# Optimization experiments

Hardware: AMD Instinct MI355X
Metric: run time of the kernel (lower is better)

The kernel has to match this reference:

```python
import jax, jax.numpy as jnp
import numpy as np

B, C, H, W = 8, 512, 64, 32
SE_MID = C // 16
BN_EPS = 1e-5


def conv1x1(x, w, b):
    # x: [B,Cin,H,W], w: [Cout,Cin], b: [Cout]
    return jnp.einsum('bchw,oc->bohw', x, w) + b[None, :, None, None]


def setup_inputs() -> dict:
    key = jax.random.key(0)
    ks = jax.random.split(key, 17)
    s = 0.05
    return {
        'x': jax.random.normal(ks[0], (B, C, H, W), jnp.float32),
        'g_w': jax.random.normal(ks[1], (1, C), jnp.float32) * s,
        'g_b': jax.random.normal(ks[2], (1,), jnp.float32) * s,
        'theta_w': jax.random.normal(ks[3], (1, C), jnp.float32) * s,
        'theta_b': jax.random.normal(ks[4], (1,), jnp.float32) * s,
        'phi_w': jax.random.normal(ks[5], (1, C), jnp.float32) * s,
        'phi_b': jax.random.normal(ks[6], (1,), jnp.float32) * s,
        'W_w': jax.random.normal(ks[7], (C, 1), jnp.float32) * s,
        'W_b': jax.random.normal(ks[8], (C,), jnp.float32) * s,
        'bn_gamma': jax.random.normal(ks[9], (C,), jnp.float32) * s + 1.0,
        'bn_beta': jax.random.normal(ks[10], (C,), jnp.float32) * s,
        'bn_mean': jax.random.normal(ks[11], (C,), jnp.float32) * s,
        'bn_var': jax.random.uniform(ks[12], (C,), jnp.float32, 0.5, 1.5),
        'se1_w': jax.random.normal(ks[13], (SE_MID, C), jnp.float32) * s,
        'se1_b': jnp.zeros((SE_MID,), jnp.float32),
        'se2_w': jax.random.normal(ks[14], (C, SE_MID), jnp.float32) * s,
        'se2_b': jnp.zeros((C,), jnp.float32),
    }


def reference(x, g_w, g_b, theta_w, theta_b, phi_w, phi_b, W_w, W_b,
              bn_gamma, bn_beta, bn_mean, bn_var, se1_w, se1_b, se2_w, se2_b):
    b, c, h, w = x.shape
    N = h * w
    # SE channel gate from global average pool: [B,C,1,1]
    x_avg = jnp.mean(x, axis=(2, 3), keepdims=True)
    se_mid = jax.nn.relu(conv1x1(x_avg, se1_w, se1_b))
    W_cw = jax.nn.sigmoid(conv1x1(se_mid, se2_w, se2_b))  # [B,C,1,1]

    # inter_channels == 1: each projection is a length-N vector per sample
    g_x = conv1x1(x, g_w, g_b).reshape(b, N)          # [B,N]
    theta_x = conv1x1(x, theta_w, theta_b).reshape(b, N)  # [B,N]
    phi_x = conv1x1(x, phi_w, phi_b).reshape(b, N)        # [B,N]

    # f[b,i,j] = theta[b,i] * phi[b,j]; row softmax over j; y = f_div_C @ g
    f = theta_x[:, :, None] * phi_x[:, None, :]       # [B,N,N]
    f_div_C = jax.nn.softmax(f, axis=-1)
    y = jnp.einsum('bij,bj->bi', f_div_C, g_x)        # [B,N]
    y = y.reshape(b, 1, h, w)

    # W: 1x1 conv (1 -> C) + BatchNorm2d (inference form with running stats)
    W_y = conv1x1(y, W_w, W_b)                        # [B,C,H,W]
    inv = bn_gamma / jnp.sqrt(bn_var + BN_EPS)
    W_y = (W_y - bn_mean[None, :, None, None]) * inv[None, :, None, None] \
          + bn_beta[None, :, None, None]

    return W_cw * W_y + x
```

## Files before the change

### kernel.cpp

```cpp
#include <hip/hip_runtime.h>

#define BB 8
#define CC 512
#define NN 2048
#define SEM 32
#define BN_EPS 1e-5f
#define LOG2E 1.4426950408889634f

#define CG 32
#define NG (CC / CG)
#define KARR (NG * BB * NN)

__global__ __launch_bounds__(256) void k1(const float* __restrict__ x,
    const float* __restrict__ gw, const float* __restrict__ tw, const float* __restrict__ pw,
    float* __restrict__ pp, float* __restrict__ avgp)
{
    int tid = threadIdx.x;
    int wave = tid >> 6, lane = tid & 63;
    int blk = blockIdx.x;
    int h = blk & 1;
    int g = (blk >> 1) & (NG - 1);
    int b = blk >> 5;
    int c0 = g * CG;

    const float2* xp = reinterpret_cast<const float2*>(x)
                     + (size_t)(b * CC + c0) * (NN / 2) + h * 512 + tid;

    float2 ag0 = {0,0}, at0 = {0,0}, ap0 = {0,0};
    float2 ag1 = {0,0}, at1 = {0,0}, ap1 = {0,0};
    float s[CG];

    #pragma unroll 8
    for (int c = 0; c < CG; ++c) {
        float2 v0 = xp[(size_t)c * (NN / 2)];
        float2 v1 = xp[(size_t)c * (NN / 2) + 256];
        float wg = gw[c0 + c], wt = tw[c0 + c], wp = pw[c0 + c];
        ag0.x = fmaf(wg, v0.x, ag0.x); ag0.y = fmaf(wg, v0.y, ag0.y);
        at0.x = fmaf(wt, v0.x, at0.x); at0.y = fmaf(wt, v0.y, at0.y);
        ap0.x = fmaf(wp, v0.x, ap0.x); ap0.y = fmaf(wp, v0.y, ap0.y);
        ag1.x = fmaf(wg, v1.x, ag1.x); ag1.y = fmaf(wg, v1.y, ag1.y);
        at1.x = fmaf(wt, v1.x, at1.x); at1.y = fmaf(wt, v1.y, at1.y);
        ap1.x = fmaf(wp, v1.x, ap1.x); ap1.y = fmaf(wp, v1.y, ap1.y);
        s[c] = (v0.x + v0.y) + (v1.x + v1.y);
    }

    size_t i0 = (size_t)(g * BB + b) * 1024 + h * 512 + tid;
    float2* pp2 = reinterpret_cast<float2*>(pp);
    pp2[i0]                  = ag0;
    pp2[i0 + 256]            = ag1;
    pp2[KARR / 2 + i0]       = at0;
    pp2[KARR / 2 + i0 + 256] = at1;
    pp2[KARR + i0]           = ap0;
    pp2[KARR + i0 + 256]     = ap1;

    #pragma unroll
    for (int o = 32; o > 0; o >>= 1) {
        #pragma unroll
        for (int c = 0; c < CG; ++c) s[c] += __shfl_down(s[c], o);
    }
    if (lane == 0) {
        #pragma unroll
        for (int c = 0; c < CG; ++c)
            avgp[(size_t)(b * CC + c0 + c) * 8 + h * 4 + wave] = s[c];
    }
}

__global__ __launch_bounds__(256) void k2(
    const float* __restrict__ pp,
    const float* __restrict__ tb, const float* __restrict__ pb,
    float* __restrict__ gx, float* __restrict__ tx, float* __restrict__ px)
{
    int tid = threadIdx.x;
    int oct = blockIdx.x & 7;
    int g3  = blockIdx.x >> 3;
    int k   = g3 % 3;
    int b   = g3 / 3;
    int p   = oct * 256 + tid;
    const float* base = pp + (size_t)k * KARR + (size_t)b * NN + p;
    float v = 0.f;
    #pragma unroll
    for (int g = 0; g < NG; ++g)
        v += base[(size_t)g * BB * NN];
    int o = b * NN + p;
    if (k == 0)      gx[o] = v;
    else if (k == 1) tx[o] = v + tb[0];
    else             px[o] = v + pb[0];
}

__global__ __launch_bounds__(256) void k3(
    const float* __restrict__ gx, const float* __restrict__ tx,
    const float* __restrict__ px, const float* __restrict__ avgp,
    const float* __restrict__ gb,
    const float* __restrict__ se1w, const float* __restrict__ se1b,
    const float* __restrict__ se2w, const float* __restrict__ se2b,
    const float* __restrict__ Ww, const float* __restrict__ Wb,
    const float* __restrict__ gamma, const float* __restrict__ beta,
    const float* __restrict__ mean, const float* __restrict__ var,
    float* __restrict__ y, float* __restrict__ Ac, float* __restrict__ Dc)
{
    __shared__ float smem[4096];
    int tid = threadIdx.x;

    if (blockIdx.x >= 1024) {
        int b = blockIdx.x - 1024;
        float* sA = smem;
        float* sP = smem + 512;
        float* sM = smem + 768;
        for (int c = tid; c < CC; c += 256) {
            const float* apt = avgp + (size_t)(b * CC + c) * 8;
            float ssum = 0.f;
            #pragma unroll
            for (int k = 0; k < 8; ++k) ssum += apt[k];
            sA[c] = ssum * (1.0f / NN);
        }
        __syncthreads();
        {
            int m = tid >> 3, sub = tid & 7;
            const float* w1 = se1w + m * CC + sub * 64;
            const float* a1 = sA + sub * 64;
            float ssum = 0.f;
            #pragma unroll
            for (int k = 0; k < 64; ++k) ssum = fmaf(a1[k], w1[k], ssum);
            sP[m * 8 + sub] = ssum;
        }
        __syncthreads();
        if (tid < SEM) {
            float t = 0.f;
            #pragma unroll
            for (int k = 0; k < 8; ++k) t += sP[tid * 8 + k];
            sM[tid] = fmaxf(t + se1b[tid], 0.f);
        }
        __syncthreads();
        float gbv = gb[0];
        for (int c = tid; c < CC; c += 256) {
            float s2 = 0.f;
            #pragma unroll
            for (int m = 0; m < SEM; ++m) s2 = fmaf(sM[m], se2w[c * SEM + m], s2);
            s2 += se2b[c];
            float wcw = 1.f / (1.f + __expf(-s2));
            float inv = gamma[c] * rsqrtf(var[c] + BN_EPS);
            float A = wcw * Ww[c] * inv;
            Ac[b * CC + c] = A;
            Dc[b * CC + c] = wcw * ((Wb[c] - mean[c]) * inv + beta[c]) + A * gbv;
        }
        return;
    }

    float* spx = smem;
    float* sgx = smem + 2048;
    int b  = blockIdx.x >> 7;
    int i0 = (blockIdx.x & 127) << 4;
    {
        const float4* pxr = reinterpret_cast<const float4*>(px + (size_t)b * NN);
        const float4* gxr = reinterpret_cast<const float4*>(gx + (size_t)b * NN);
        float4* spx4 = reinterpret_cast<float4*>(spx);
        float4* sgx4 = reinterpret_cast<float4*>(sgx);
        #pragma unroll
        for (int w = 0; w < 2; ++w) {
            int idx = w * 256 + tid;
            spx4[idx] = pxr[idx];
            sgx4[idx] = gxr[idx];
        }
    }
    __syncthreads();

    int wave = tid >> 6, lane = tid & 63;
    int r0 = i0 + wave * 4;
    float t0 = tx[b * NN + r0 + 0] * LOG2E;
    float t1 = tx[b * NN + r0 + 1] * LOG2E;
    float t2 = tx[b * NN + r0 + 2] * LOG2E;
    float t3 = tx[b * NN + r0 + 3] * LOG2E;
    float s0 = 0.f, g0 = 0.f, s1 = 0.f, g1 = 0.f;
    float s2 = 0.f, g2 = 0.f, s3 = 0.f, g3 = 0.f;
    const float2* spx2 = reinterpret_cast<const float2*>(spx);
    const float2* sgx2 = reinterpret_cast<const float2*>(sgx);
    #pragma unroll 4
    for (int it = 0; it < 16; ++it) {
        int jj = it * 64 + lane;
        float2 xv = spx2[jj];
        float2 gv = sgx2[jj];
        float e0a = exp2f(fminf(t0 * xv.x, 115.f)), e0b = exp2f(fminf(t0 * xv.y, 115.f));
        float e1a = exp2f(fminf(t1 * xv.x, 115.f)), e1b = exp2f(fminf(t1 * xv.y, 115.f));
        float e2a = exp2f(fminf(t2 * xv.x, 115.f)), e2b = exp2f(fminf(t2 * xv.y, 115.f));
        float e3a = exp2f(fminf(t3 * xv.x, 115.f)), e3b = exp2f(fminf(t3 * xv.y, 115.f));
        s0 += e0a + e0b; g0 = fmaf(e0a, gv.x, fmaf(e0b, gv.y, g0));
        s1 += e1a + e1b; g1 = fmaf(e1a, gv.x, fmaf(e1b, gv.y, g1));
        s2 += e2a + e2b; g2 = fmaf(e2a, gv.x, fmaf(e2b, gv.y, g2));
        s3 += e3a + e3b; g3 = fmaf(e3a, gv.x, fmaf(e3b, gv.y, g3));
    }
    for (int o = 32; o > 0; o >>= 1) {
        s0 += __shfl_down(s0, o); g0 += __shfl_down(g0, o);
        s1 += __shfl_down(s1, o); g1 += __shfl_down(g1, o);
        s2 += __shfl_down(s2, o); g2 += __shfl_down(g2, o);
        s3 += __shfl_down(s3, o); g3 += __shfl_down(g3, o);
    }
    if (lane == 0) {
        y[b * NN + r0 + 0] = g0 / s0;
        y[b * NN + r0 + 1] = g1 / s1;
        y[b * NN + r0 + 2] = g2 / s2;
        y[b * NN + r0 + 3] = g3 / s3;
    }
}

__global__ __launch_bounds__(256) void k4(
    const float* __restrict__ x, const float* __restrict__ y,
    const float* __restrict__ Ac, const float* __restrict__ Dc,
    float* __restrict__ out)
{
    int bc = blockIdx.x;
    int b = bc >> 9;
    float a = Ac[bc], d = Dc[bc];
    const float4* x4 = reinterpret_cast<const float4*>(x) + (size_t)bc * (NN / 4);
    const float4* y4 = reinterpret_cast<const float4*>(y) + (size_t)b * (NN / 4);
    float4* o4 = reinterpret_cast<float4*>(out) + (size_t)bc * (NN / 4);
    int tid = threadIdx.x;
    #pragma unroll
    for (int k = 0; k < 2; ++k) {
        int idx = k * 256 + tid;
        float4 xv = x4[idx], yv = y4[idx], ov;
        ov.x = fmaf(a, yv.x, d) + xv.x;
        ov.y = fmaf(a, yv.y, d) + xv.y;
        ov.z = fmaf(a, yv.z, d) + xv.z;
        ov.w = fmaf(a, yv.w, d) + xv.w;
        o4[idx] = ov;
    }
}

extern "C" void kernel_launch(void* const* d_in, const int* in_sizes, int n_in,
                              void* d_out, int out_size, void* d_ws, size_t ws_size,
                              hipStream_t stream) {
    const float* x    = (const float*)d_in[0];
    const float* gw   = (const float*)d_in[1];
    const float* gb   = (const float*)d_in[2];
    const float* tw   = (const float*)d_in[3];
    const float* tb   = (const float*)d_in[4];
    const float* pw   = (const float*)d_in[5];
    const float* pb   = (const float*)d_in[6];
    const float* Ww   = (const float*)d_in[7];
    const float* Wb   = (const float*)d_in[8];
    const float* gam  = (const float*)d_in[9];
    const float* bet  = (const float*)d_in[10];
    const float* mu   = (const float*)d_in[11];
    const float* var  = (const float*)d_in[12];
    const float* se1w = (const float*)d_in[13];
    const float* se1b = (const float*)d_in[14];
    const float* se2w = (const float*)d_in[15];
    const float* se2b = (const float*)d_in[16];

    float* ws   = (float*)d_ws;
    float* pp   = ws; ws += 3 * (size_t)KARR;
    float* avgp = ws; ws += BB * CC * 8;
    float* gx   = ws; ws += BB * NN;
    float* tx   = ws; ws += BB * NN;
    float* px   = ws; ws += BB * NN;
    float* y    = ws; ws += BB * NN;
    float* Ac   = ws; ws += BB * CC;
    float* Dc   = ws; ws += BB * CC;
    float* out  = (float*)d_out;

    k1<<<BB * NG * 2, 256, 0, stream>>>(x, gw, tw, pw, pp, avgp);
    k2<<<BB * 3 * 8, 256, 0, stream>>>(pp, tb, pb, gx, tx, px);
    k3<<<1024 + BB, 256, 0, stream>>>(gx, tx, px, avgp, gb, se1w, se1b, se2w, se2b,
                                      Ww, Wb, gam, bet, mu, var, y, Ac, Dc);
    k4<<<BB * CC, 256, 0, stream>>>(x, y, Ac, Dc, out);
}
```

Measured before the change: 43.92 us.

## Replace partial-sum buffer and reduce kernel with global atomics in k1

The projection kernel now adds its per-channel-group partial sums for g, theta, phi and the channel averages straight into zeroed output buffers with atomicAdd. This removes the intermediate partial buffer and the separate reduction kernel, at the cost of a memset launch and atomic contention. The theta/phi biases are folded into k3, k1 is re-tiled to 16 channels and 4 spatial quarters per block, and the final output uses nontemporal stores. Floating-point summation order becomes nondeterministic.

```diff
diff --git a/kernel.cpp b/kernel.cpp
--- a/kernel.cpp
+++ b/kernel.cpp
@@ -7,90 +7,57 @@
 #define BN_EPS 1e-5f
 #define LOG2E 1.4426950408889634f
 
-#define CG 32
-#define NG (CC / CG)
-#define KARR (NG * BB * NN)
+typedef float floatx4 __attribute__((ext_vector_type(4)));
 
 __global__ __launch_bounds__(256) void k1(const float* __restrict__ x,
     const float* __restrict__ gw, const float* __restrict__ tw, const float* __restrict__ pw,
-    float* __restrict__ pp, float* __restrict__ avgp)
+    float* __restrict__ gxa, float* __restrict__ txa, float* __restrict__ pxa,
+    float* __restrict__ avg)
 {
     int tid = threadIdx.x;
-    int wave = tid >> 6, lane = tid & 63;
+    int lane = tid & 63;
     int blk = blockIdx.x;
-    int h = blk & 1;
-    int g = (blk >> 1) & (NG - 1);
-    int b = blk >> 5;
-    int c0 = g * CG;
+    int q = blk & 3;
+    int g = (blk >> 2) & 31;
+    int b = blk >> 7;
+    int c0 = g * 16;
 
     const float2* xp = reinterpret_cast<const float2*>(x)
-                     + (size_t)(b * CC + c0) * (NN / 2) + h * 512 + tid;
-
-    float2 ag0 = {0,0}, at0 = {0,0}, ap0 = {0,0};
-    float2 ag1 = {0,0}, at1 = {0,0}, ap1 = {0,0};
-    float s[CG];
-
-    #pragma unroll 8
-    for (int c = 0; c < CG; ++c) {
-        float2 v0 = xp[(size_t)c * (NN / 2)];
-        float2 v1 = xp[(size_t)c * (NN / 2) + 256];
+                     + (size_t)(b * CC + c0) * (NN / 2) + q * 256 + tid;
+
+    float2 ag = {0,0}, at_ = {0,0}, ap = {0,0};
+    float s[16];
+    #pragma unroll
+    for (int c = 0; c < 16; ++c) {
+        float2 v = xp[(size_t)c * (NN / 2)];
         float wg = gw[c0 + c], wt = tw[c0 + c], wp = pw[c0 + c];
-        ag0.x = fmaf(wg, v0.x, ag0.x); ag0.y = fmaf(wg, v0.y, ag0.y);
-        at0.x = fmaf(wt, v0.x, at0.x); at0.y = fmaf(wt, v0.y, at0.y);
-        ap0.x = fmaf(wp, v0.x, ap0.x); ap0.y = fmaf(wp, v0.y, ap0.y);
-        ag1.x = fmaf(wg, v1.x, ag1.x); ag1.y = fmaf(wg, v1.y, ag1.y);
-        at1.x = fmaf(wt, v1.x, at1.x); at1.y = fmaf(wt, v1.y, at1.y);
-        ap1.x = fmaf(wp, v1.x, ap1.x); ap1.y = fmaf(wp, v1.y, ap1.y);
-        s[c] = (v0.x + v0.y) + (v1.x + v1.y);
-    }
-
-    size_t i0 = (size_t)(g * BB + b) * 1024 + h * 512 + tid;
-    float2* pp2 = reinterpret_cast<float2*>(pp);
-    pp2[i0]                  = ag0;
-    pp2[i0 + 256]            = ag1;
-    pp2[KARR / 2 + i0]       = at0;
-    pp2[KARR / 2 + i0 + 256] = at1;
-    pp2[KARR + i0]           = ap0;
-    pp2[KARR + i0 + 256]     = ap1;
+        ag.x  = fmaf(wg, v.x, ag.x);  ag.y  = fmaf(wg, v.y, ag.y);
+        at_.x = fmaf(wt, v.x, at_.x); at_.y = fmaf(wt, v.y, at_.y);
+        ap.x  = fmaf(wp, v.x, ap.x);  ap.y  = fmaf(wp, v.y, ap.y);
+        s[c] = v.x + v.y;
+    }
+
+    int p = b * NN + q * 512 + tid * 2;
+    atomicAdd(&gxa[p],     ag.x);  atomicAdd(&gxa[p + 1], ag.y);
+    atomicAdd(&txa[p],     at_.x); atomicAdd(&txa[p + 1], at_.y);
+    atomicAdd(&pxa[p],     ap.x);  atomicAdd(&pxa[p + 1], ap.y);
 
     #pragma unroll
     for (int o = 32; o > 0; o >>= 1) {
         #pragma unroll
-        for (int c = 0; c < CG; ++c) s[c] += __shfl_down(s[c], o);
+        for (int c = 0; c < 16; ++c) s[c] += __shfl_down(s[c], o);
     }
     if (lane == 0) {
         #pragma unroll
-        for (int c = 0; c < CG; ++c)
-            avgp[(size_t)(b * CC + c0 + c) * 8 + h * 4 + wave] = s[c];
-    }
-}
-
-__global__ __launch_bounds__(256) void k2(
-    const float* __restrict__ pp,
-    const float* __restrict__ tb, const float* __restrict__ pb,
-    float* __restrict__ gx, float* __restrict__ tx, float* __restrict__ px)
-{
-    int tid = threadIdx.x;
-    int oct = blockIdx.x & 7;
-    int g3  = blockIdx.x >> 3;
-    int k   = g3 % 3;
-    int b   = g3 / 3;
-    int p   = oct * 256 + tid;
-    const float* base = pp + (size_t)k * KARR + (size_t)b * NN + p;
-    float v = 0.f;
-    #pragma unroll
-    for (int g = 0; g < NG; ++g)
-        v += base[(size_t)g * BB * NN];
-    int o = b * NN + p;
-    if (k == 0)      gx[o] = v;
-    else if (k == 1) tx[o] = v + tb[0];
-    else             px[o] = v + pb[0];
+        for (int c = 0; c < 16; ++c)
+            atomicAdd(&avg[b * CC + c0 + c], s[c]);
+    }
 }
 
 __global__ __launch_bounds__(256) void k3(
     const float* __restrict__ gx, const float* __restrict__ tx,
-    const float* __restrict__ px, const float* __restrict__ avgp,
-    const float* __restrict__ gb,
+    const float* __restrict__ px, const float* __restrict__ avg,
+    const float* __restrict__ gb, const float* __restrict__ tb, const float* __restrict__ pb,
     const float* __restrict__ se1w, const float* __restrict__ se1b,
     const float* __restrict__ se2w, const float* __restrict__ se2b,
     const float* __restrict__ Ww, const float* __restrict__ Wb,
@@ -106,13 +73,8 @@
         float* sA = smem;
         float* sP = smem + 512;
         float* sM = smem + 768;
-        for (int c = tid; c < CC; c += 256) {
-            const float* apt = avgp + (size_t)(b * CC + c) * 8;
-            float ssum = 0.f;
-            #pragma unroll
-            for (int k = 0; k < 8; ++k) ssum += apt[k];
-            sA[c] = ssum * (1.0f / NN);
-        }
+        for (int c = tid; c < CC; c += 256)
+            sA[c] = avg[b * CC + c] * (1.0f / NN);
         __syncthreads();
         {
             int m = tid >> 3, sub = tid & 7;
@@ -150,6 +112,7 @@
     float* sgx = smem + 2048;
     int b  = blockIdx.x >> 7;
     int i0 = (blockIdx.x & 127) << 4;
+    float pbv = pb[0], tbv = tb[0];
     {
         const float4* pxr = reinterpret_cast<const float4*>(px + (size_t)b * NN);
         const float4* gxr = reinterpret_cast<const float4*>(gx + (size_t)b * NN);
@@ -158,7 +121,9 @@
         #pragma unroll
         for (int w = 0; w < 2; ++w) {
             int idx = w * 256 + tid;
-            spx4[idx] = pxr[idx];
+            float4 pv = pxr[idx];
+            pv.x += pbv; pv.y += pbv; pv.z += pbv; pv.w += pbv;
+            spx4[idx] = pv;
             sgx4[idx] = gxr[idx];
         }
     }
@@ -166,10 +131,10 @@
 
     int wave = tid >> 6, lane = tid & 63;
     int r0 = i0 + wave * 4;
-    float t0 = tx[b * NN + r0 + 0] * LOG2E;
-    float t1 = tx[b * NN + r0 + 1] * LOG2E;
-    float t2 = tx[b * NN + r0 + 2] * LOG2E;
-    float t3 = tx[b * NN + r0 + 3] * LOG2E;
+    float t0 = (tx[b * NN + r0 + 0] + tbv) * LOG2E;
+    float t1 = (tx[b * NN + r0 + 1] + tbv) * LOG2E;
+    float t2 = (tx[b * NN + r0 + 2] + tbv) * LOG2E;
+    float t3 = (tx[b * NN + r0 + 3] + tbv) * LOG2E;
     float s0 = 0.f, g0 = 0.f, s1 = 0.f, g1 = 0.f;
     float s2 = 0.f, g2 = 0.f, s3 = 0.f, g3 = 0.f;
     const float2* spx2 = reinterpret_cast<const float2*>(spx);
@@ -212,17 +177,18 @@
     float a = Ac[bc], d = Dc[bc];
     const float4* x4 = reinterpret_cast<const float4*>(x) + (size_t)bc * (NN / 4);
     const float4* y4 = reinterpret_cast<const float4*>(y) + (size_t)b * (NN / 4);
-    float4* o4 = reinterpret_cast<float4*>(out) + (size_t)bc * (NN / 4);
+    floatx4* o4 = reinterpret_cast<floatx4*>(out) + (size_t)bc * (NN / 4);
     int tid = threadIdx.x;
     #pragma unroll
     for (int k = 0; k < 2; ++k) {
         int idx = k * 256 + tid;
-        float4 xv = x4[idx], yv = y4[idx], ov;
+        float4 xv = x4[idx], yv = y4[idx];
+        floatx4 ov;
         ov.x = fmaf(a, yv.x, d) + xv.x;
         ov.y = fmaf(a, yv.y, d) + xv.y;
         ov.z = fmaf(a, yv.z, d) + xv.z;
         ov.w = fmaf(a, yv.w, d) + xv.w;
-        o4[idx] = ov;
+        __builtin_nontemporal_store(ov, &o4[idx]);
     }
 }
 
@@ -247,20 +213,22 @@
     const float* se2w = (const float*)d_in[15];
     const float* se2b = (const float*)d_in[16];
 
-    float* ws   = (float*)d_ws;
-    float* pp   = ws; ws += 3 * (size_t)KARR;
-    float* avgp = ws; ws += BB * CC * 8;
-    float* gx   = ws; ws += BB * NN;
-    float* tx   = ws; ws += BB * NN;
-    float* px   = ws; ws += BB * NN;
-    float* y    = ws; ws += BB * NN;
-    float* Ac   = ws; ws += BB * CC;
-    float* Dc   = ws; ws += BB * CC;
-    float* out  = (float*)d_out;
-
-    k1<<<BB * NG * 2, 256, 0, stream>>>(x, gw, tw, pw, pp, avgp);
-    k2<<<BB * 3 * 8, 256, 0, stream>>>(pp, tb, pb, gx, tx, px);
-    k3<<<1024 + BB, 256, 0, stream>>>(gx, tx, px, avgp, gb, se1w, se1b, se2w, se2b,
+    float* ws  = (float*)d_ws;
+    float* gxa = ws; ws += BB * NN;
+    float* txa = ws; ws += BB * NN;
+    float* pxa = ws; ws += BB * NN;
+    float* avg = ws; ws += BB * CC;
+    float* y   = ws; ws += BB * NN;
+    float* Ac  = ws; ws += BB * CC;
+    float* Dc  = ws; ws += BB * CC;
+    float* out = (float*)d_out;
+
+    size_t zbytes = (size_t)(3 * BB * NN + BB * CC) * sizeof(float);
+    (void)hipMemsetAsync((void*)gxa, 0, zbytes, stream);
+
+    k1<<<1024, 256, 0, stream>>>(x, gw, tw, pw, gxa, txa, pxa, avg);
+    k3<<<1024 + BB, 256, 0, stream>>>(gxa, txa, pxa, avg, gb, tb, pb,
+                                      se1w, se1b, se2w, se2b,
                                       Ww, Wb, gam, bet, mu, var, y, Ac, Dc);
     k4<<<BB * CC, 256, 0, stream>>>(x, y, Ac, Dc, out);
 }
```

After: 58.57 us. 33.3% more time.

## Split k1 into finer channel/pixel tiles, move SE gate into k2, nontemporal output stores

Applied to the files above, without the earlier changes.

The projection kernel now uses 16-channel groups and quarter-row pixel slices, launching 1024 blocks instead of 256. It also issues all loads up front, which is meant to raise memory-level parallelism and occupancy. The SE/BN coefficient computation moves from the attention kernel into the partial-sum reduction kernel, so the attention kernel becomes uniform. The final kernel writes its output with nontemporal stores to avoid polluting the cache. In exchange, there are twice as many partial sums for k2 to reduce and a larger avgp workspace.

```diff
diff --git a/kernel.cpp b/kernel.cpp
--- a/kernel.cpp
+++ b/kernel.cpp
@@ -7,145 +7,141 @@
 #define BN_EPS 1e-5f
 #define LOG2E 1.4426950408889634f
 
-#define CG 32
-#define NG (CC / CG)
+#define NCC 16
+#define NG (CC / NCC)
 #define KARR (NG * BB * NN)
 
-__global__ __launch_bounds__(256) void k1(const float* __restrict__ x,
+typedef float floatx4 __attribute__((ext_vector_type(4)));
+
+__global__ __launch_bounds__(256, 4) void k1(const float* __restrict__ x,
     const float* __restrict__ gw, const float* __restrict__ tw, const float* __restrict__ pw,
     float* __restrict__ pp, float* __restrict__ avgp)
 {
     int tid = threadIdx.x;
     int wave = tid >> 6, lane = tid & 63;
     int blk = blockIdx.x;
-    int h = blk & 1;
-    int g = (blk >> 1) & (NG - 1);
-    int b = blk >> 5;
-    int c0 = g * CG;
+    int q = blk & 3;
+    int g = (blk >> 2) & (NG - 1);
+    int b = blk >> 7;
+    int c0 = g * NCC;
 
     const float2* xp = reinterpret_cast<const float2*>(x)
-                     + (size_t)(b * CC + c0) * (NN / 2) + h * 512 + tid;
-
-    float2 ag0 = {0,0}, at0 = {0,0}, ap0 = {0,0};
-    float2 ag1 = {0,0}, at1 = {0,0}, ap1 = {0,0};
-    float s[CG];
-
-    #pragma unroll 8
-    for (int c = 0; c < CG; ++c) {
-        float2 v0 = xp[(size_t)c * (NN / 2)];
-        float2 v1 = xp[(size_t)c * (NN / 2) + 256];
+                     + (size_t)(b * CC + c0) * (NN / 2) + q * 256 + tid;
+
+    float2 v[NCC];
+    #pragma unroll
+    for (int c = 0; c < NCC; ++c)
+        v[c] = xp[(size_t)c * (NN / 2)];
+
+    float2 ag = {0,0}, at_ = {0,0}, ap = {0,0};
+    float s[NCC];
+    #pragma unroll
+    for (int c = 0; c < NCC; ++c) {
         float wg = gw[c0 + c], wt = tw[c0 + c], wp = pw[c0 + c];
-        ag0.x = fmaf(wg, v0.x, ag0.x); ag0.y = fmaf(wg, v0.y, ag0.y);
-        at0.x = fmaf(wt, v0.x, at0.x); at0.y = fmaf(wt, v0.y, at0.y);
-        ap0.x = fmaf(wp, v0.x, ap0.x); ap0.y = fmaf(wp, v0.y, ap0.y);
-        ag1.x = fmaf(wg, v1.x, ag1.x); ag1.y = fmaf(wg, v1.y, ag1.y);
-        at1.x = fmaf(wt, v1.x, at1.x); at1.y = fmaf(wt, v1.y, at1.y);
-        ap1.x = fmaf(wp, v1.x, ap1.x); ap1.y = fmaf(wp, v1.y, ap1.y);
-        s[c] = (v0.x + v0.y) + (v1.x + v1.y);
-    }
-
-    size_t i0 = (size_t)(g * BB + b) * 1024 + h * 512 + tid;
+        ag.x  = fmaf(wg, v[c].x, ag.x);  ag.y  = fmaf(wg, v[c].y, ag.y);
+        at_.x = fmaf(wt, v[c].x, at_.x); at_.y = fmaf(wt, v[c].y, at_.y);
+        ap.x  = fmaf(wp, v[c].x, ap.x);  ap.y  = fmaf(wp, v[c].y, ap.y);
+        s[c] = v[c].x + v[c].y;
+    }
+
+    size_t base2 = (size_t)(g * BB + b) * (NN / 2) + q * 256 + tid;
     float2* pp2 = reinterpret_cast<float2*>(pp);
-    pp2[i0]                  = ag0;
-    pp2[i0 + 256]            = ag1;
-    pp2[KARR / 2 + i0]       = at0;
-    pp2[KARR / 2 + i0 + 256] = at1;
-    pp2[KARR + i0]           = ap0;
-    pp2[KARR + i0 + 256]     = ap1;
+    pp2[base2]            = ag;
+    pp2[base2 + KARR / 2] = at_;
+    pp2[base2 + KARR]     = ap;
 
     #pragma unroll
     for (int o = 32; o > 0; o >>= 1) {
         #pragma unroll
-        for (int c = 0; c < CG; ++c) s[c] += __shfl_down(s[c], o);
+        for (int c = 0; c < NCC; ++c) s[c] += __shfl_down(s[c], o);
     }
     if (lane == 0) {
         #pragma unroll
-        for (int c = 0; c < CG; ++c)
-            avgp[(size_t)(b * CC + c0 + c) * 8 + h * 4 + wave] = s[c];
+        for (int c = 0; c < NCC; ++c)
+            avgp[(size_t)(b * CC + c0 + c) * 16 + q * 4 + wave] = s[c];
     }
 }
 
 __global__ __launch_bounds__(256) void k2(
-    const float* __restrict__ pp,
-    const float* __restrict__ tb, const float* __restrict__ pb,
-    float* __restrict__ gx, float* __restrict__ tx, float* __restrict__ px)
-{
-    int tid = threadIdx.x;
-    int oct = blockIdx.x & 7;
-    int g3  = blockIdx.x >> 3;
-    int k   = g3 % 3;
-    int b   = g3 / 3;
-    int p   = oct * 256 + tid;
-    const float* base = pp + (size_t)k * KARR + (size_t)b * NN + p;
-    float v = 0.f;
-    #pragma unroll
-    for (int g = 0; g < NG; ++g)
-        v += base[(size_t)g * BB * NN];
-    int o = b * NN + p;
-    if (k == 0)      gx[o] = v;
-    else if (k == 1) tx[o] = v + tb[0];
-    else             px[o] = v + pb[0];
-}
-
-__global__ __launch_bounds__(256) void k3(
-    const float* __restrict__ gx, const float* __restrict__ tx,
-    const float* __restrict__ px, const float* __restrict__ avgp,
-    const float* __restrict__ gb,
+    const float* __restrict__ pp, const float* __restrict__ avgp,
+    const float* __restrict__ gb, const float* __restrict__ tb, const float* __restrict__ pb,
     const float* __restrict__ se1w, const float* __restrict__ se1b,
     const float* __restrict__ se2w, const float* __restrict__ se2b,
     const float* __restrict__ Ww, const float* __restrict__ Wb,
     const float* __restrict__ gamma, const float* __restrict__ beta,
     const float* __restrict__ mean, const float* __restrict__ var,
-    float* __restrict__ y, float* __restrict__ Ac, float* __restrict__ Dc)
+    float* __restrict__ gx, float* __restrict__ tx, float* __restrict__ px,
+    float* __restrict__ Ac, float* __restrict__ Dc)
+{
+    int tid = threadIdx.x;
+    if (blockIdx.x < 192) {
+        int oct = blockIdx.x & 7;
+        int g3  = blockIdx.x >> 3;
+        int k   = g3 % 3;
+        int b   = g3 / 3;
+        int p   = oct * 256 + tid;
+        const float* base = pp + (size_t)k * KARR + (size_t)b * NN + p;
+        float v = 0.f;
+        #pragma unroll
+        for (int g = 0; g < NG; ++g)
+            v += base[(size_t)g * BB * NN];
+        int o = b * NN + p;
+        if (k == 0)      gx[o] = v;
+        else if (k == 1) tx[o] = v + tb[0];
+        else             px[o] = v + pb[0];
+        return;
+    }
+
+    __shared__ float smem[1024];
+    int b = blockIdx.x - 192;
+    float* sA = smem;
+    float* sP = smem + 512;
+    float* sM = smem + 768;
+    for (int c = tid; c < CC; c += 256) {
+        const float* apt = avgp + (size_t)(b * CC + c) * 16;
+        float ssum = 0.f;
+        #pragma unroll
+        for (int k = 0; k < 16; ++k) ssum += apt[k];
+        sA[c] = ssum * (1.0f / NN);
+    }
+    __syncthreads();
+    {
+        int m = tid >> 3, sub = tid & 7;
+        const float* w1 = se1w + m * CC + sub * 64;
+        const float* a1 = sA + sub * 64;
+        float ssum = 0.f;
+        #pragma unroll
+        for (int k = 0; k < 64; ++k) ssum = fmaf(a1[k], w1[k], ssum);
+        sP[m * 8 + sub] = ssum;
+    }
+    __syncthreads();
+    if (tid < SEM) {
+        float t = 0.f;
+        #pragma unroll
+        for (int k = 0; k < 8; ++k) t += sP[tid * 8 + k];
+        sM[tid] = fmaxf(t + se1b[tid], 0.f);
+    }
+    __syncthreads();
+    float gbv = gb[0];
+    for (int c = tid; c < CC; c += 256) {
+        float s2 = 0.f;
+        #pragma unroll
+        for (int m = 0; m < SEM; ++m) s2 = fmaf(sM[m], se2w[c * SEM + m], s2);
+        s2 += se2b[c];
+        float wcw = 1.f / (1.f + __expf(-s2));
+        float inv = gamma[c] * rsqrtf(var[c] + BN_EPS);
+        float A = wcw * Ww[c] * inv;
+        Ac[b * CC + c] = A;
+        Dc[b * CC + c] = wcw * ((Wb[c] - mean[c]) * inv + beta[c]) + A * gbv;
+    }
+}
+
+__global__ __launch_bounds__(256) void k3(
+    const float* __restrict__ gx, const float* __restrict__ tx,
+    const float* __restrict__ px, float* __restrict__ y)
 {
     __shared__ float smem[4096];
     int tid = threadIdx.x;
-
-    if (blockIdx.x >= 1024) {
-        int b = blockIdx.x - 1024;
-        float* sA = smem;
-        float* sP = smem + 512;
-        float* sM = smem + 768;
-        for (int c = tid; c < CC; c += 256) {
-            const float* apt = avgp + (size_t)(b * CC + c) * 8;
-            float ssum = 0.f;
-            #pragma unroll
-            for (int k = 0; k < 8; ++k) ssum += apt[k];
-            sA[c] = ssum * (1.0f / NN);
-        }
-        __syncthreads();
-        {
-            int m = tid >> 3, sub = tid & 7;
-            const float* w1 = se1w + m * CC + sub * 64;
-            const float* a1 = sA + sub * 64;
-            float ssum = 0.f;
-            #pragma unroll
-            for (int k = 0; k < 64; ++k) ssum = fmaf(a1[k], w1[k], ssum);
-            sP[m * 8 + sub] = ssum;
-        }
-        __syncthreads();
-        if (tid < SEM) {
-            float t = 0.f;
-            #pragma unroll
-            for (int k = 0; k < 8; ++k) t += sP[tid * 8 + k];
-            sM[tid] = fmaxf(t + se1b[tid], 0.f);
-        }
-        __syncthreads();
-        float gbv = gb[0];
-        for (int c = tid; c < CC; c += 256) {
-            float s2 = 0.f;
-            #pragma unroll
-            for (int m = 0; m < SEM; ++m) s2 = fmaf(sM[m], se2w[c * SEM + m], s2);
-            s2 += se2b[c];
-            float wcw = 1.f / (1.f + __expf(-s2));
-            float inv = gamma[c] * rsqrtf(var[c] + BN_EPS);
-            float A = wcw * Ww[c] * inv;
-            Ac[b * CC + c] = A;
-            Dc[b * CC + c] = wcw * ((Wb[c] - mean[c]) * inv + beta[c]) + A * gbv;
-        }
-        return;
-    }
-
     float* spx = smem;
     float* sgx = smem + 2048;
     int b  = blockIdx.x >> 7;
@@ -212,17 +208,18 @@
     float a = Ac[bc], d = Dc[bc];
     const float4* x4 = reinterpret_cast<const float4*>(x) + (size_t)bc * (NN / 4);
     const float4* y4 = reinterpret_cast<const float4*>(y) + (size_t)b * (NN / 4);
-    float4* o4 = reinterpret_cast<float4*>(out) + (size_t)bc * (NN / 4);
+    floatx4* o4 = reinterpret_cast<floatx4*>(out) + (size_t)bc * (NN / 4);
     int tid = threadIdx.x;
     #pragma unroll
     for (int k = 0; k < 2; ++k) {
         int idx = k * 256 + tid;
-        float4 xv = x4[idx], yv = y4[idx], ov;
+        float4 xv = x4[idx], yv = y4[idx];
+        floatx4 ov;
         ov.x = fmaf(a, yv.x, d) + xv.x;
         ov.y = fmaf(a, yv.y, d) + xv.y;
         ov.z = fmaf(a, yv.z, d) + xv.z;
         ov.w = fmaf(a, yv.w, d) + xv.w;
-        o4[idx] = ov;
+        __builtin_nontemporal_store(ov, &o4[idx]);
     }
 }
 
@@ -249,7 +246,7 @@
 
     float* ws   = (float*)d_ws;
     float* pp   = ws; ws += 3 * (size_t)KARR;
-    float* avgp = ws; ws += BB * CC * 8;
+    float* avgp = ws; ws += BB * CC * 16;
     float* gx   = ws; ws += BB * NN;
     float* tx   = ws; ws += BB * NN;
     float* px   = ws; ws += BB * NN;
@@ -258,9 +255,9 @@
     float* Dc   = ws; ws += BB * CC;
     float* out  = (float*)d_out;
 
-    k1<<<BB * NG * 2, 256, 0, stream>>>(x, gw, tw, pw, pp, avgp);
-    k2<<<BB * 3 * 8, 256, 0, stream>>>(pp, tb, pb, gx, tx, px);
-    k3<<<1024 + BB, 256, 0, stream>>>(gx, tx, px, avgp, gb, se1w, se1b, se2w, se2b,
-                                      Ww, Wb, gam, bet, mu, var, y, Ac, Dc);
+    k1<<<1024, 256, 0, stream>>>(x, gw, tw, pw, pp, avgp);
+    k2<<<200, 256, 0, stream>>>(pp, avgp, gb, tb, pb, se1w, se1b, se2w, se2b,
+                                Ww, Wb, gam, bet, mu, var, gx, tx, px, Ac, Dc);
+    k3<<<1024, 256, 0, stream>>>(gx, tx, px, y);
     k4<<<BB * CC, 256, 0, stream>>>(x, y, Ac, Dc, out);
 }
```

Measured after the change: 43.91 us. Within noise of the previous version (-0.0%).
